# Performance work log

Measured on AMD Instinct MI355X. Metric: run time of the kernel, lower is better.

Reference implementation:

```python
import jax, jax.numpy as jnp
import numpy as np

B, N, G = 16, 6000, 256
T = 200                     # TRAIN_ROIS_PER_IMAGE
RATIO = 0.33                # POSITIVE_ROI_RATIO
POS_NUM = int(T * RATIO)    # 66 positive slots
NEG_SLOTS = T - POS_NUM     # 134 negative slots
BBOX_STD = jnp.asarray([0.1, 0.1, 0.2, 0.2], jnp.float32)
EPS = 1e-8


def _rand_boxes(key, b, n):
    # valid [y1,x1,y2,x2] boxes in [0,1]
    k1, k2 = jax.random.split(key)
    tl = jax.random.uniform(k1, (b, n, 2)) * 0.7
    wh = jax.random.uniform(k2, (b, n, 2)) * 0.25 + 0.02
    return jnp.concatenate([tl, tl + wh], axis=-1).astype(jnp.float32)


def setup_inputs() -> dict:
    key = jax.random.key(0)
    k1, k2, k3, k4, k5 = jax.random.split(key, 5)
    rois = _rand_boxes(k1, B, N)
    rois = rois.at[:, N - 1000:].set(0.0)          # zero padding tail (remove_zero_padding)
    gt_boxes = _rand_boxes(k2, B, G)
    gt_ids = jax.random.randint(k3, (B, G), 1, 81, dtype=jnp.int32)
    gt_ids = gt_ids.at[:, G - 32:G - 16].set(-1)   # crowd boxes (ids < 0)
    gt_ids = gt_ids.at[:, G - 16:].set(0)          # padded gt
    gt_boxes = gt_boxes.at[:, G - 16:].set(0.0)
    pos_score = jax.random.uniform(k4, (B, N), dtype=jnp.float32)
    neg_score = jax.random.uniform(k5, (B, N), dtype=jnp.float32)
    return {"rois": rois, "gt_ids": gt_ids, "gt_boxes": gt_boxes,
            "pos_score": pos_score, "neg_score": neg_score}


def _pairwise_iou(a, b):
    # a:[N,4], b:[G,4] -> [N,G]
    y1 = jnp.maximum(a[:, None, 0], b[None, :, 0])
    x1 = jnp.maximum(a[:, None, 1], b[None, :, 1])
    y2 = jnp.minimum(a[:, None, 2], b[None, :, 2])
    x2 = jnp.minimum(a[:, None, 3], b[None, :, 3])
    inter = jnp.clip(y2 - y1, 0.0) * jnp.clip(x2 - x1, 0.0)
    area_a = (a[:, 2] - a[:, 0]) * (a[:, 3] - a[:, 1])
    area_b = (b[:, 2] - b[:, 0]) * (b[:, 3] - b[:, 1])
    union = area_a[:, None] + area_b[None, :] - inter
    return inter / jnp.maximum(union, EPS)


def _bbox_offset(boxes, gt):
    h = jnp.maximum(boxes[:, 2] - boxes[:, 0], EPS)
    w = jnp.maximum(boxes[:, 3] - boxes[:, 1], EPS)
    cy = boxes[:, 0] + 0.5 * h
    cx = boxes[:, 1] + 0.5 * w
    gh = jnp.maximum(gt[:, 2] - gt[:, 0], EPS)
    gw = jnp.maximum(gt[:, 3] - gt[:, 1], EPS)
    gcy = gt[:, 0] + 0.5 * gh
    gcx = gt[:, 1] + 0.5 * gw
    off = jnp.stack([(gcy - cy) / h, (gcx - cx) / w,
                     jnp.log(gh / h), jnp.log(gw / w)], axis=1)
    return off / BBOX_STD


def _per_image(rois, gt_ids, gt_boxes, pos_score, neg_score):
    roi_valid = jnp.any(rois != 0.0, axis=1)        # [N]
    gt_valid = jnp.any(gt_boxes != 0.0, axis=1)     # [G]
    crowd = gt_valid & (gt_ids < 0)
    non_crowd = gt_valid & (gt_ids > 0)

    iou = _pairwise_iou(rois, gt_boxes)             # [N,G]
    iou_nc = jnp.where(non_crowd[None, :], iou, -1.0)
    iou_nc_max = jnp.max(iou_nc, axis=1)
    iou_cr_max = jnp.max(jnp.where(crowd[None, :], iou, 0.0), axis=1)

    pos_mask = roi_valid & (iou_nc_max >= 0.5)
    neg_mask = roi_valid & (iou_nc_max < 0.5) & (iou_cr_max < 0.001)

    # random sampling == sort by iid uniform scores (masked out -> -inf)
    pos_idx = jnp.argsort(-jnp.where(pos_mask, pos_score, -jnp.inf))[:POS_NUM]
    pos_count = jnp.minimum(jnp.sum(pos_mask), POS_NUM).astype(jnp.int32)
    pos_slot_valid = jnp.arange(POS_NUM) < pos_count

    neg_target = (jnp.float32(1.0 / RATIO) * pos_count.astype(jnp.float32)).astype(jnp.int32) - pos_count
    neg_idx = jnp.argsort(-jnp.where(neg_mask, neg_score, -jnp.inf))[:NEG_SLOTS]
    neg_count = jnp.minimum(jnp.sum(neg_mask).astype(jnp.int32),
                            jnp.minimum(neg_target, NEG_SLOTS))
    neg_slot_valid = jnp.arange(NEG_SLOTS) < neg_count

    pos_rois_raw = rois[pos_idx]                                   # [P,4]
    pos_rois = jnp.where(pos_slot_valid[:, None], pos_rois_raw, 0.0)
    neg_rois = jnp.where(neg_slot_valid[:, None], rois[neg_idx], 0.0)

    assign = jnp.argmax(iou_nc[pos_idx], axis=1)                   # gt assignment
    roi_gt_boxes = gt_boxes[assign]
    roi_gt_ids = jnp.where(pos_slot_valid, gt_ids[assign], 0)

    off = _bbox_offset(pos_rois_raw, roi_gt_boxes)
    off = jnp.where(pos_slot_valid[:, None], off, 0.0)

    out_rois = jnp.concatenate([pos_rois, neg_rois], axis=0)       # [T,4]
    out_ids = jnp.pad(roi_gt_ids, (0, NEG_SLOTS))                  # [T]
    out_off = jnp.pad(off, ((0, NEG_SLOTS), (0, 0)))               # [T,4]
    return out_rois, out_ids, out_off


def reference(rois, gt_ids, gt_boxes, pos_score, neg_score):
    return jax.vmap(_per_image)(rois, gt_ids, gt_boxes, pos_score, neg_score)
```

## Files before the change

kernel.cpp:

```cpp
#include <hip/hip_runtime.h>

#define BIMG 16
#define NROI 6000
#define NGT  256
#define TPOS 66
#define TNEG 134
#define TTOT 200
#define EPSF 1e-8f
#define INVALID_SCORE 0xFFFFFFFFu

#define CPB 4
#define UNITSB 47
#define P1_BLOCKS (UNITSB * BIMG)
#define NWAIT (2 * BIMG)
#define NT 256
#define SLOTS 24
#define CAND_CAP 384

#define MAGIC1 0x9E3779B9u
#define MAGIC2 0x85EBCA77u

typedef unsigned long long u64;
typedef unsigned int u32;
typedef unsigned char u8;

struct P1Shared {
    float4 ncbox[NGT];
    float2 ncai[NGT];
    float4 crbox[NGT];
    float  crarea[NGT];
    int nccnt, crcnt;
};

struct SelShared {
    u32 hist[2048];
    u32 wtot[4];
    u32 wsuf[4];
    int pick;
    u32 higher;
    u32 pickpop;
    u32 count;
    u64 comp[CAND_CAP];
    int cnt;
    int sel[TNEG];
};

__device__ __forceinline__ void phase1_block(
    int unit,
    const float* __restrict__ rois, const int* __restrict__ gt_ids,
    const float* __restrict__ gt_boxes, const float* __restrict__ pos_score,
    const float* __restrict__ neg_score, u32* __restrict__ pos_s,
    u32* __restrict__ neg_s, u32* __restrict__ assign, u32* __restrict__ flags,
    P1Shared& S)
{
#pragma clang fp contract(off)
    const int b = unit / UNITSB;
    const int u = unit - b * UNITSB;

    if (threadIdx.x == 0) { S.nccnt = 0; S.crcnt = 0; }
    __syncthreads();
    {
        const int g = threadIdx.x;
        float4 gb = ((const float4*)gt_boxes)[b * NGT + g];
        bool valid = (gb.x != 0.f) || (gb.y != 0.f) || (gb.z != 0.f) || (gb.w != 0.f);
        int id = gt_ids[b * NGT + g];
        float area = (gb.z - gb.x) * (gb.w - gb.y);
        if (valid && id > 0) {
            int slot = atomicAdd(&S.nccnt, 1);
            S.ncbox[slot] = gb;
            S.ncai[slot] = make_float2(area, (float)g);
        } else if (valid && id < 0) {
            int slot = atomicAdd(&S.crcnt, 1);
            S.crbox[slot] = gb;
            S.crarea[slot] = area;
        }
    }
    __syncthreads();
    const int nccnt = S.nccnt;
    const int crcnt = S.crcnt;

    const int r_local = threadIdx.x >> 3;
    const int sub = threadIdx.x & 7;

    for (int k = 0; k < CPB; ++k) {
        const int n = (u * CPB + k) * 32 + r_local;
        const int n_eff = min(n, NROI - 1);

        float4 rb = ((const float4*)rois)[b * NROI + n_eff];
        const bool rvalid = (rb.x != 0.f) || (rb.y != 0.f) || (rb.z != 0.f) || (rb.w != 0.f);
        const float area_a = (rb.z - rb.x) * (rb.w - rb.y);

        float best = -1.0f;
        float bestg = 0.0f;
        float crmax = 0.0f;

        for (int i = sub; i < nccnt; i += 8) {
            float4 p0 = S.ncbox[i];
            float2 ai = S.ncai[i];
            float y1 = fmaxf(rb.x, p0.x);
            float x1 = fmaxf(rb.y, p0.y);
            float y2 = fminf(rb.z, p0.z);
            float x2 = fminf(rb.w, p0.w);
            float ih = fmaxf(y2 - y1, 0.0f);
            float iw = fmaxf(x2 - x1, 0.0f);
            float inter = ih * iw;
            float uni = fmaxf(area_a + ai.x - inter, EPSF);
            float iou = inter / uni;
            bool better = (iou > best) || ((iou == best) && (ai.y < bestg));
            if (better) { best = iou; bestg = ai.y; }
        }
        for (int i = sub; i < crcnt; i += 8) {
            float4 p0 = S.crbox[i];
            float y1 = fmaxf(rb.x, p0.x);
            float x1 = fmaxf(rb.y, p0.y);
            float y2 = fminf(rb.z, p0.z);
            float x2 = fminf(rb.w, p0.w);
            float ih = fmaxf(y2 - y1, 0.0f);
            float iw = fmaxf(x2 - x1, 0.0f);
            float inter = ih * iw;
            float uni = fmaxf(area_a + S.crarea[i] - inter, EPSF);
            crmax = fmaxf(crmax, inter / uni);
        }

        for (int m = 1; m <= 4; m <<= 1) {
            float ov = __shfl_xor(best, m);
            float og = __shfl_xor(bestg, m);
            float oc = __shfl_xor(crmax, m);
            if ((ov > best) || ((ov == best) && (og < bestg))) { best = ov; bestg = og; }
            crmax = fmaxf(crmax, oc);
        }

        if (sub == 0 && n < NROI) {
            u32 ps = INVALID_SCORE, ns = INVALID_SCORE;
            if (rvalid) {
                if (best >= 0.5f)
                    ps = __float_as_uint(pos_score[b * NROI + n]);
                if ((best < 0.5f) && (crmax < 0.001f))
                    ns = __float_as_uint(neg_score[b * NROI + n]);
            }
            __hip_atomic_store(&pos_s[b * NROI + n], ps,
                               __ATOMIC_RELAXED, __HIP_MEMORY_SCOPE_AGENT);
            __hip_atomic_store(&neg_s[b * NROI + n], ns,
                               __ATOMIC_RELAXED, __HIP_MEMORY_SCOPE_AGENT);
            __hip_atomic_store(&assign[b * NROI + n], (u32)(int)bestg,
                               __ATOMIC_RELAXED, __HIP_MEMORY_SCOPE_AGENT);
        }
    }

    __syncthreads();
    if (threadIdx.x == 0) {
        __hip_atomic_store(&flags[2 * unit],     MAGIC1,
                           __ATOMIC_RELAXED, __HIP_MEMORY_SCOPE_AGENT);
        __hip_atomic_store(&flags[2 * unit + 1], MAGIC2,
                           __ATOMIC_RELAXED, __HIP_MEMORY_SCOPE_AGENT);
    }
}

__device__ __forceinline__ int count_valid(const u32* __restrict__ src,
                                           int tid, int lane, SelShared* S)
{
    int myvalid = 0;
    for (int s = 0; s < SLOTS; ++s) {
        int idx = s * NT + tid;
        myvalid += (idx < NROI && src[idx] != INVALID_SCORE);
    }
    for (int off = 1; off < 64; off <<= 1) myvalid += __shfl_xor(myvalid, off);
    if (tid == 0) S->count = 0;
    __syncthreads();
    if (lane == 0) atomicAdd(&S->count, (u32)myvalid);
    __syncthreads();
    int tot = (int)S->count;
    __syncthreads();
    return tot;
}

__device__ __forceinline__ int radix_select(const u32* __restrict__ src, int K,
                                            int tid, int lane, int w, SelShared* S)
{
    int myvalid = 0;
    for (int s = 0; s < SLOTS; ++s) {
        int idx = s * NT + tid;
        myvalid += (idx < NROI && src[idx] != INVALID_SCORE);
    }
    for (int off = 1; off < 64; off <<= 1) myvalid += __shfl_xor(myvalid, off);
    if (tid == 0) S->count = 0;
    __syncthreads();
    if (lane == 0) atomicAdd(&S->count, (u32)myvalid);
    __syncthreads();
    const int total = (int)S->count;
    const int K0 = min(K, total);
    if (K0 <= 0) return total;

    int Krem = K0;
    u64 prefix = 0ull, mask = 0ull;
    int cand = total;

    for (int p = 3; p >= 0; --p) {
        if (cand <= CAND_CAP) break;
        const int shift = p * 11;
        for (int i = tid; i < 2048; i += NT) S->hist[i] = 0;
        __syncthreads();
        for (int s = 0; s < SLOTS; ++s) {
            int idx = s * NT + tid;
            if (idx < NROI) {
                u32 v = src[idx];
                if (v != INVALID_SCORE) {
                    u64 k = ((u64)v << 13) | (u64)(8191 - idx);
                    if ((k & mask) == prefix)
                        atomicAdd(&S->hist[(u32)(k >> shift) & 2047u], 1u);
                }
            }
        }
        __syncthreads();
        u32 local = 0;
#pragma unroll
        for (int j = 0; j < 8; ++j) local += S->hist[8 * tid + j];
        u32 suf = local;
        for (int off = 1; off < 64; off <<= 1) {
            u32 v = __shfl_down(suf, off);
            if (lane + off < 64) suf += v;
        }
        if (lane == 0) S->wtot[w] = suf;
        __syncthreads();
        if (tid < 4) {
            u32 t = 0;
            for (int j = tid + 1; j < 4; ++j) t += S->wtot[j];
            S->wsuf[tid] = t;
        }
        __syncthreads();
        u32 Sincl = suf + S->wsuf[w];
        for (int k2 = 0; k2 < 8; ++k2) {
            u32 h = S->hist[8 * tid + k2];
            u32 Snext = Sincl - h;
            if (Sincl >= (u32)Krem && Snext < (u32)Krem) {
                S->pick = 8 * tid + k2;
                S->higher = Snext;
                S->pickpop = h;
            }
            Sincl = Snext;
        }
        __syncthreads();
        prefix |= ((u64)(u32)S->pick) << shift;
        mask   |= (2047ull << shift);
        Krem   -= (int)S->higher;
        cand    = (K0 - Krem) + (int)S->pickpop;
        __syncthreads();
    }

    if (tid == 0) S->cnt = 0;
    __syncthreads();
    for (int s = 0; s < SLOTS; ++s) {
        int idx = s * NT + tid;
        if (idx < NROI) {
            u32 v = src[idx];
            if (v != INVALID_SCORE) {
                u64 k = ((u64)v << 13) | (u64)(8191 - idx);
                if ((k & mask) >= prefix) {
                    int pos = atomicAdd(&S->cnt, 1);
                    S->comp[pos] = k;
                }
            }
        }
    }
    __syncthreads();
    const int Cnt = S->cnt;
    for (int c0 = tid; c0 < Cnt; c0 += NT) {
        u64 k = S->comp[c0];
        int rank = 0;
        for (int j = 0; j < Cnt; ++j) rank += (S->comp[j] > k);
        if (rank < K0) S->sel[rank] = 8191 - (int)(k & 8191ull);
    }
    __syncthreads();
    return total;
}

__device__ __forceinline__ void phase2_block(
    int wbid,
    const float* __restrict__ rois, const int* __restrict__ gt_ids,
    const float* __restrict__ gt_boxes, const u32* __restrict__ pos_s,
    const u32* __restrict__ neg_s, const u32* __restrict__ assign,
    const u32* __restrict__ flags, float* __restrict__ out, SelShared& S)
{
#pragma clang fp contract(off)
    __shared__ int s_ndone;
    const int b = wbid >> 1;
    const int side = wbid & 1;
    const int tid = threadIdx.x;
    const int lane = tid & 63;
    const int w = tid >> 6;

    const u32* fb = flags + 2 * (b * UNITSB);
    int mydone = (tid < UNITSB) ? 0 : 1;
    for (;;) {
        if (tid == 0) s_ndone = 0;
        __syncthreads();
        if (!mydone) {
            u32 a = __hip_atomic_load(&fb[2 * tid],
                                      __ATOMIC_RELAXED, __HIP_MEMORY_SCOPE_AGENT);
            u32 c = __hip_atomic_load(&fb[2 * tid + 1],
                                      __ATOMIC_RELAXED, __HIP_MEMORY_SCOPE_AGENT);
            mydone = (a == MAGIC1 && c == MAGIC2);
        }
        int d = mydone;
        for (int off = 1; off < 64; off <<= 1) d += __shfl_xor(d, off);
        if (lane == 0) atomicAdd(&s_ndone, d);
        __syncthreads();
        if (s_ndone == NT) break;
        __builtin_amdgcn_s_sleep(16);
    }
    if (tid == 0)
        (void)__hip_atomic_load(&fb[0], __ATOMIC_ACQUIRE, __HIP_MEMORY_SCOPE_AGENT);
    __syncthreads();

    float* out_rois = out;
    float* out_ids  = out + BIMG * TTOT * 4;
    float* out_off  = out + BIMG * TTOT * 4 + BIMG * TTOT;

    if (side == 0) {
        const int pos_total = radix_select(pos_s + (size_t)b * NROI, TPOS,
                                           tid, lane, w, &S);
        const int pos_count = min(pos_total, TPOS);

        if (tid < TPOS) {
            const int base = b * TTOT + tid;
            float4 ro  = make_float4(0.f, 0.f, 0.f, 0.f);
            float  idv = 0.f;
            float4 off = make_float4(0.f, 0.f, 0.f, 0.f);
            if (tid < pos_count) {
                int n = S.sel[tid];
                float4 rb = ((const float4*)rois)[b * NROI + n];
                ro = rb;
                int g = (int)assign[b * NROI + n];
                float4 gb = ((const float4*)gt_boxes)[b * NGT + g];
                idv = (float)gt_ids[b * NGT + g];

                float h  = fmaxf(rb.z - rb.x, EPSF);
                float wd = fmaxf(rb.w - rb.y, EPSF);
                float cy = rb.x + 0.5f * h;
                float cx = rb.y + 0.5f * wd;
                float gh = fmaxf(gb.z - gb.x, EPSF);
                float gw = fmaxf(gb.w - gb.y, EPSF);
                float gcy = gb.x + 0.5f * gh;
                float gcx = gb.y + 0.5f * gw;
                off.x = ((gcy - cy) / h)  / 0.1f;
                off.y = ((gcx - cx) / wd) / 0.1f;
                off.z = logf(gh / h)  / 0.2f;
                off.w = logf(gw / wd) / 0.2f;
            }
            ((float4*)out_rois)[base] = ro;
            out_ids[base] = idv;
            ((float4*)out_off)[base] = off;
        }
    } else {
        const int pos_total = count_valid(pos_s + (size_t)b * NROI, tid, lane, &S);
        const int pos_count = min(pos_total, TPOS);
        const float ratio_inv = (float)(1.0 / 0.33);
        const int neg_target = (int)(ratio_inv * (float)pos_count) - pos_count;

        const int neg_total = radix_select(neg_s + (size_t)b * NROI, TNEG,
                                           tid, lane, w, &S);
        const int neg_count = max(0, min(neg_total, min(neg_target, TNEG)));

        if (tid < TNEG) {
            const int base = b * TTOT + TPOS + tid;
            float4 ro = make_float4(0.f, 0.f, 0.f, 0.f);
            if (tid < neg_count) {
                int n = S.sel[tid];
                ro = ((const float4*)rois)[b * NROI + n];
            }
            ((float4*)out_rois)[base] = ro;
            out_ids[base] = 0.f;
            ((float4*)out_off)[base] = make_float4(0.f, 0.f, 0.f, 0.f);
        }
    }
}

__global__ __launch_bounds__(NT, 4)
void fused_kernel(const float* __restrict__ rois,
                  const int* __restrict__ gt_ids,
                  const float* __restrict__ gt_boxes,
                  const float* __restrict__ pos_score,
                  const float* __restrict__ neg_score,
                  u32* __restrict__ pos_s,
                  u32* __restrict__ neg_s,
                  u32* __restrict__ assign,
                  u32* __restrict__ flags,
                  float* __restrict__ out)
{
    constexpr size_t SB = sizeof(P1Shared) > sizeof(SelShared)
                        ? sizeof(P1Shared) : sizeof(SelShared);
    __shared__ __align__(16) char smem[SB];

    if (blockIdx.x >= NWAIT) {
        phase1_block((int)blockIdx.x - NWAIT, rois, gt_ids, gt_boxes, pos_score,
                     neg_score, pos_s, neg_s, assign, flags,
                     *reinterpret_cast<P1Shared*>(smem));
    } else {
        phase2_block((int)blockIdx.x, rois, gt_ids, gt_boxes,
                     pos_s, neg_s, assign, flags, out,
                     *reinterpret_cast<SelShared*>(smem));
    }
}

extern "C" void kernel_launch(void* const* d_in, const int* in_sizes, int n_in,
                              void* d_out, int out_size, void* d_ws, size_t ws_size,
                              hipStream_t stream) {
    const float* rois      = (const float*)d_in[0];
    const int*   gt_ids    = (const int*)d_in[1];
    const float* gt_boxes  = (const float*)d_in[2];
    const float* pos_score = (const float*)d_in[3];
    const float* neg_score = (const float*)d_in[4];
    float* out = (float*)d_out;

    char* ws = (char*)d_ws;
    u32* pos_s  = (u32*)(ws + 0);
    u32* neg_s  = (u32*)(ws + 384000);
    u32* assign = (u32*)(ws + 768000);
    u32* flags  = (u32*)(ws + 1152000);

    fused_kernel<<<NWAIT + P1_BLOCKS, NT, 0, stream>>>(
        rois, gt_ids, gt_boxes, pos_score, neg_score,
        pos_s, neg_s, assign, flags, out);
}
```

Before: 103.4 us.

## Halve ROIs per block, ballot-compact GT lists, recompute areas, raise occupancy

Phase-1 blocks now handle 2 ROI chunks instead of 4, doubling the block count per image so more blocks run in parallel. GT compaction uses wave ballots and prefix counts instead of shared atomics, which keeps slots in original GT order so the argmax tie-break can compare slot indices and map back through a u16 table. GT areas are recomputed in the loop instead of being stored, which shrinks shared memory. Launch bounds request 8 blocks per SM, which may increase register pressure.

```diff
diff --git a/kernel.cpp b/kernel.cpp
--- a/kernel.cpp
+++ b/kernel.cpp
@@ -9,8 +9,8 @@
 #define EPSF 1e-8f
 #define INVALID_SCORE 0xFFFFFFFFu
 
-#define CPB 4
-#define UNITSB 47
+#define CPB 2
+#define UNITSB 94
 #define P1_BLOCKS (UNITSB * BIMG)
 #define NWAIT (2 * BIMG)
 #define NT 256
@@ -22,14 +22,13 @@
 
 typedef unsigned long long u64;
 typedef unsigned int u32;
-typedef unsigned char u8;
+typedef unsigned short u16;
 
 struct P1Shared {
     float4 ncbox[NGT];
-    float2 ncai[NGT];
     float4 crbox[NGT];
-    float  crarea[NGT];
-    int nccnt, crcnt;
+    u16    gmap[NGT];
+    int    wnc[4], wcr[4];
 };
 
 struct SelShared {
@@ -57,27 +56,34 @@
     const int b = unit / UNITSB;
     const int u = unit - b * UNITSB;
 
-    if (threadIdx.x == 0) { S.nccnt = 0; S.crcnt = 0; }
-    __syncthreads();
     {
         const int g = threadIdx.x;
+        const int lane = g & 63, w = g >> 6;
         float4 gb = ((const float4*)gt_boxes)[b * NGT + g];
         bool valid = (gb.x != 0.f) || (gb.y != 0.f) || (gb.z != 0.f) || (gb.w != 0.f);
         int id = gt_ids[b * NGT + g];
-        float area = (gb.z - gb.x) * (gb.w - gb.y);
-        if (valid && id > 0) {
-            int slot = atomicAdd(&S.nccnt, 1);
+        bool isnc = valid && (id > 0);
+        bool iscr = valid && (id < 0);
+        u64 mnc = __ballot(isnc);
+        u64 mcr = __ballot(iscr);
+        if (lane == 0) { S.wnc[w] = (int)__popcll(mnc); S.wcr[w] = (int)__popcll(mcr); }
+        __syncthreads();
+        int offnc = 0, offcr = 0;
+        for (int j = 0; j < w; ++j) { offnc += S.wnc[j]; offcr += S.wcr[j]; }
+        u64 below = (lane == 0) ? 0ull : (~0ull >> (64 - lane));
+        if (isnc) {
+            int slot = offnc + (int)__popcll(mnc & below);
             S.ncbox[slot] = gb;
-            S.ncai[slot] = make_float2(area, (float)g);
-        } else if (valid && id < 0) {
-            int slot = atomicAdd(&S.crcnt, 1);
+            S.gmap[slot] = (u16)g;
+        }
+        if (iscr) {
+            int slot = offcr + (int)__popcll(mcr & below);
             S.crbox[slot] = gb;
-            S.crarea[slot] = area;
-        }
-    }
-    __syncthreads();
-    const int nccnt = S.nccnt;
-    const int crcnt = S.crcnt;
+        }
+    }
+    __syncthreads();
+    const int nccnt = S.wnc[0] + S.wnc[1] + S.wnc[2] + S.wnc[3];
+    const int crcnt = S.wcr[0] + S.wcr[1] + S.wcr[2] + S.wcr[3];
 
     const int r_local = threadIdx.x >> 3;
     const int sub = threadIdx.x & 7;
@@ -91,12 +97,11 @@
         const float area_a = (rb.z - rb.x) * (rb.w - rb.y);
 
         float best = -1.0f;
-        float bestg = 0.0f;
+        float bsl  = 0.0f;
         float crmax = 0.0f;
 
         for (int i = sub; i < nccnt; i += 8) {
             float4 p0 = S.ncbox[i];
-            float2 ai = S.ncai[i];
             float y1 = fmaxf(rb.x, p0.x);
             float x1 = fmaxf(rb.y, p0.y);
             float y2 = fminf(rb.z, p0.z);
@@ -104,10 +109,10 @@
             float ih = fmaxf(y2 - y1, 0.0f);
             float iw = fmaxf(x2 - x1, 0.0f);
             float inter = ih * iw;
-            float uni = fmaxf(area_a + ai.x - inter, EPSF);
+            float area_b = (p0.z - p0.x) * (p0.w - p0.y);
+            float uni = fmaxf(area_a + area_b - inter, EPSF);
             float iou = inter / uni;
-            bool better = (iou > best) || ((iou == best) && (ai.y < bestg));
-            if (better) { best = iou; bestg = ai.y; }
+            if (iou > best) { best = iou; bsl = (float)i; }
         }
         for (int i = sub; i < crcnt; i += 8) {
             float4 p0 = S.crbox[i];
@@ -118,15 +123,16 @@
             float ih = fmaxf(y2 - y1, 0.0f);
             float iw = fmaxf(x2 - x1, 0.0f);
             float inter = ih * iw;
-            float uni = fmaxf(area_a + S.crarea[i] - inter, EPSF);
+            float area_b = (p0.z - p0.x) * (p0.w - p0.y);
+            float uni = fmaxf(area_a + area_b - inter, EPSF);
             crmax = fmaxf(crmax, inter / uni);
         }
 
         for (int m = 1; m <= 4; m <<= 1) {
             float ov = __shfl_xor(best, m);
-            float og = __shfl_xor(bestg, m);
+            float os = __shfl_xor(bsl, m);
             float oc = __shfl_xor(crmax, m);
-            if ((ov > best) || ((ov == best) && (og < bestg))) { best = ov; bestg = og; }
+            if ((ov > best) || ((ov == best) && (os < bsl))) { best = ov; bsl = os; }
             crmax = fmaxf(crmax, oc);
         }
 
@@ -138,11 +144,12 @@
                 if ((best < 0.5f) && (crmax < 0.001f))
                     ns = __float_as_uint(neg_score[b * NROI + n]);
             }
+            int gsel = (nccnt > 0) ? (int)S.gmap[(int)bsl] : 0;
             __hip_atomic_store(&pos_s[b * NROI + n], ps,
                                __ATOMIC_RELAXED, __HIP_MEMORY_SCOPE_AGENT);
             __hip_atomic_store(&neg_s[b * NROI + n], ns,
                                __ATOMIC_RELAXED, __HIP_MEMORY_SCOPE_AGENT);
-            __hip_atomic_store(&assign[b * NROI + n], (u32)(int)bestg,
+            __hip_atomic_store(&assign[b * NROI + n], (u32)gsel,
                                __ATOMIC_RELAXED, __HIP_MEMORY_SCOPE_AGENT);
         }
     }
@@ -375,7 +382,7 @@
     }
 }
 
-__global__ __launch_bounds__(NT, 4)
+__global__ __launch_bounds__(NT, 8)
 void fused_kernel(const float* __restrict__ rois,
                   const int* __restrict__ gt_ids,
                   const float* __restrict__ gt_boxes,
```

Measured after the change: 120.3 us. +16.3%, slower.
